# Performance work log

Hardware: AMD Instinct MI355X
Metric: run time of the kernel (lower is better)

Reference implementation:

```python
import jax, jax.numpy as jnp
import numpy as np

N, M, D = 1024, 1024, 512


def setup_inputs() -> dict:
    key = jax.random.key(0)
    ks = jax.random.split(key, 12)
    s = 1.0 / np.sqrt(D)
    return {
        "q": jax.random.normal(ks[0], (N, D), jnp.float32),
        "k": jax.random.normal(ks[1], (M, D), jnp.float32),
        "v": jax.random.normal(ks[2], (M, D), jnp.float32),
        "mask": jax.random.randint(ks[3], (N, M), 0, 2) > 0,
        "Wq": jax.random.normal(ks[4], (D, D), jnp.float32) * s,
        "bq": jax.random.normal(ks[5], (D,), jnp.float32) * s,
        "Wk": jax.random.normal(ks[6], (D, D), jnp.float32) * s,
        "bk": jax.random.normal(ks[7], (D,), jnp.float32) * s,
        "Wv": jax.random.normal(ks[8], (D, D), jnp.float32) * s,
        "bv": jax.random.normal(ks[9], (D,), jnp.float32) * s,
        "Ww": jax.random.normal(ks[10], (D,), jnp.float32) * s,
        "bw": jax.random.normal(ks[11], (1,), jnp.float32) * s,
    }


def reference(q, k, v, mask, Wq, bq, Wk, bk, Wv, bv, Ww, bw):
    # Linear projections (torch Linear: x @ W.T + b)
    qp = q @ Wq.T + bq  # [N, D]
    kp = k @ Wk.T + bk  # [M, D]
    vp = v @ Wv.T + bv  # [M, D]
    # Bahdanau additive score: W(tanh(q_n + k_m)) -> [N, M]
    h = jnp.tanh(qp[:, None, :] + kp[None, :, :])  # [N, M, D]
    scores = jnp.einsum('nmd,d->nm', h, Ww) + bw[0]
    scores = jnp.where(mask, scores, jnp.float32(-1000000.0))
    attn = jax.nn.softmax(scores, axis=1)  # softmax over M (dim 1)
    context = jnp.einsum('nm,md->nd', attn, vp)  # [N, D]
    return context
```

## Files before the change

### kernel.cpp

```cpp
#include <hip/hip_runtime.h>
#include <hip/hip_bf16.h>
#include <float.h>


#define NROWS 1024
#define DDIM  512
#define MDIM  1024

typedef __attribute__((ext_vector_type(8))) short s8v;
typedef __attribute__((ext_vector_type(4))) float f4v;
typedef __attribute__((ext_vector_type(2))) float v2f;

__device__ __forceinline__ float bf2f(ushort h) {
    return __uint_as_float(((unsigned)h) << 16);
}
__device__ __forceinline__ ushort2 f2bf2(float a, float b) {
    __hip_bfloat162 t = __float22bfloat162_rn(float2{a, b});
    union { __hip_bfloat162 v; ushort2 u; } c; c.v = t;
    return c.u;
}
__device__ __forceinline__ void hl2(float a, float b, ushort2& h, ushort2& l) {
    h = f2bf2(a, b);
    l = f2bf2(a - bf2f(h.x), b - bf2f(h.y));
}

__global__ __launch_bounds__(256) void proj_gemm(
    const float* __restrict__ q, const float* __restrict__ kk_,
    const float* __restrict__ v,
    const float* __restrict__ Wq, const float* __restrict__ bq,
    const float* __restrict__ Wk, const float* __restrict__ bk,
    const float* __restrict__ Wv, const float* __restrict__ bv,
    float* __restrict__ eq, float* __restrict__ ekT,
    ushort* __restrict__ vph, ushort* __restrict__ vpl,
    float* __restrict__ S, float CS)
{
    __shared__ ushort Ah[4096], Al[4096], Bh[4096], Bl[4096];

    const float* A; const float* B; const float* bias;
    int biasRow;
    if (blockIdx.z == 0)      { A = q;   B = Wq;  bias = bq; biasRow = 0; }
    else if (blockIdx.z == 1) { A = Wk;  B = kk_; bias = bk; biasRow = 1; }
    else                      { A = Wv;  B = v;   bias = bv; biasRow = 1; }

    const int bi = (blockIdx.z == 0) ? blockIdx.x : blockIdx.y;
    const int bj = (blockIdx.z == 0) ? blockIdx.y : blockIdx.x;

    const int t    = threadIdx.x;
    const int lane = t & 63;
    const int w    = t >> 6;
    const int lm   = lane & 15;
    const int lq   = lane >> 4;
    const int i0   = bi * 64;
    const int j0   = bj * 64;
    const int mh   = (w >> 1) * 32;
    const int nh   = (w & 1) * 32;

    if (blockIdx.z == 0) {
        const int jb = blockIdx.x * 8 + blockIdx.y;
        float4 zz = {0.f, 0.f, 0.f, 0.f};
#pragma unroll
        for (int p = 0; p < 8; ++p)
            *(float4*)&S[(size_t)jb * 8192 + (t + p * 256) * 4] = zz;
    }

    f4v acc[2][2] = {{{0.f,0.f,0.f,0.f},{0.f,0.f,0.f,0.f}},
                     {{0.f,0.f,0.f,0.f},{0.f,0.f,0.f,0.f}}};
    float4 pa[4], pb[4];

    const int sr = t >> 4, sc4 = t & 15;
#pragma unroll
    for (int p = 0; p < 4; ++p) {
        int r = sr + p * 16;
        pa[p] = *(const float4*)&A[(size_t)(i0 + r) * DDIM + sc4 * 4];
        pb[p] = *(const float4*)&B[(size_t)(j0 + r) * DDIM + sc4 * 4];
    }

    for (int kc = 0; kc < 8; ++kc) {
        __syncthreads();
#pragma unroll
        for (int p = 0; p < 4; ++p) {
            int r = sr + p * 16;
            int ad = r * 64 + (((sc4 >> 1) ^ (r & 7)) << 3) + (sc4 & 1) * 4;
            ushort2 h01, l01, h23, l23;
            hl2(pa[p].x, pa[p].y, h01, l01);
            hl2(pa[p].z, pa[p].w, h23, l23);
            ushort4 ha = {h01.x, h01.y, h23.x, h23.y};
            ushort4 la = {l01.x, l01.y, l23.x, l23.y};
            *(ushort4*)&Ah[ad] = ha;
            *(ushort4*)&Al[ad] = la;
            hl2(pb[p].x, pb[p].y, h01, l01);
            hl2(pb[p].z, pb[p].w, h23, l23);
            ushort4 hb = {h01.x, h01.y, h23.x, h23.y};
            ushort4 lb = {l01.x, l01.y, l23.x, l23.y};
            *(ushort4*)&Bh[ad] = hb;
            *(ushort4*)&Bl[ad] = lb;
        }
        __syncthreads();
        if (kc < 7) {
            const int k0 = (kc + 1) * 64;
#pragma unroll
            for (int p = 0; p < 4; ++p) {
                int r = sr + p * 16;
                pa[p] = *(const float4*)&A[(size_t)(i0 + r) * DDIM + k0 + sc4 * 4];
                pb[p] = *(const float4*)&B[(size_t)(j0 + r) * DDIM + k0 + sc4 * 4];
            }
        }
#pragma unroll
        for (int ks = 0; ks < 2; ++ks) {
            const int kb = ks * 4 + lq;
            s8v afh[2], afl[2], bfh[2], bfl[2];
#pragma unroll
            for (int g = 0; g < 2; ++g) {
                int ra = mh + g * 16 + lm;
                int rb = nh + g * 16 + lm;
                int aa = ra * 64 + ((kb ^ (ra & 7)) << 3);
                int ab = rb * 64 + ((kb ^ (rb & 7)) << 3);
                afh[g] = *(const s8v*)&Ah[aa];
                afl[g] = *(const s8v*)&Al[aa];
                bfh[g] = *(const s8v*)&Bh[ab];
                bfl[g] = *(const s8v*)&Bl[ab];
            }
#pragma unroll
            for (int mi = 0; mi < 2; ++mi)
#pragma unroll
                for (int ni = 0; ni < 2; ++ni) {
                    acc[mi][ni] = __builtin_amdgcn_mfma_f32_16x16x32_bf16(
                        afh[mi], bfh[ni], acc[mi][ni], 0, 0, 0);
                    acc[mi][ni] = __builtin_amdgcn_mfma_f32_16x16x32_bf16(
                        afh[mi], bfl[ni], acc[mi][ni], 0, 0, 0);
                    acc[mi][ni] = __builtin_amdgcn_mfma_f32_16x16x32_bf16(
                        afl[mi], bfh[ni], acc[mi][ni], 0, 0, 0);
                }
        }
    }

    const float CLAMP = 8192.0f;
    const float SCw   = 1.220703125e-4f;
#pragma unroll
    for (int mi = 0; mi < 2; ++mi) {
#pragma unroll
        for (int ni = 0; ni < 2; ++ni) {
#pragma unroll
            for (int p = 0; p < 4; ++p) {
                int row = i0 + mh + mi * 16 + lq * 4 + p;
                int col = j0 + nh + ni * 16 + lm;
                float val = acc[mi][ni][p] + (biasRow ? bias[row] : bias[col]);
                if (blockIdx.z == 0) {
                    eq[(size_t)row * 512 + col] =
                        fminf(__builtin_amdgcn_exp2f(val * CS), CLAMP) * SCw;
                } else if (blockIdx.z == 1) {
                    ekT[(size_t)row * 1024 + col] =
                        fminf(__builtin_amdgcn_exp2f(val * CS), CLAMP);
                } else {
                    ushort2 h2 = f2bf2(val, val);
                    vph[(size_t)row * 1024 + col] = h2.x;
                    ushort2 l2 = f2bf2(val - bf2f(h2.x), 0.f);
                    vpl[(size_t)row * 1024 + col] = l2.x;
                }
            }
        }
    }
}

#define SMCH 128

#define TREE8(K0,K1,K2,K3,K4,K5,K6,K7,DCQ)                                     \
    {                                                                          \
        float4 wgA = *(const float4*)&wws[(DCQ)];                              \
        float4 wgB = *(const float4*)&wws[(DCQ) + 4];                          \
        _Pragma("unroll")                                                      \
        for (int nn = 0; nn < 4; ++nn) {                                       \
            float4 egA = *(const float4*)&es[(wrow + nn) * 128 + (DCQ)];       \
            float4 egB = *(const float4*)&es[(wrow + nn) * 128 + (DCQ) + 4];   \
            v2f A0 = __builtin_elementwise_fma(K0, (v2f){egA.x, egA.x}, cc2);  \
            v2f A1 = __builtin_elementwise_fma(K1, (v2f){egA.y, egA.y}, cc2);  \
            v2f A2 = __builtin_elementwise_fma(K2, (v2f){egA.z, egA.z}, cc2);  \
            v2f A3 = __builtin_elementwise_fma(K3, (v2f){egA.w, egA.w}, cc2);  \
            v2f A4 = __builtin_elementwise_fma(K4, (v2f){egB.x, egB.x}, cc2);  \
            v2f A5 = __builtin_elementwise_fma(K5, (v2f){egB.y, egB.y}, cc2);  \
            v2f A6 = __builtin_elementwise_fma(K6, (v2f){egB.z, egB.z}, cc2);  \
            v2f A7 = __builtin_elementwise_fma(K7, (v2f){egB.w, egB.w}, cc2);  \
            v2f n01 = __builtin_elementwise_fma((v2f){wgA.y, wgA.y}, A0,       \
                                                (v2f){wgA.x, wgA.x} * A1);     \
            v2f d01 = A0 * A1;                                                 \
            v2f n23 = __builtin_elementwise_fma((v2f){wgA.w, wgA.w}, A2,       \
                                                (v2f){wgA.z, wgA.z} * A3);     \
            v2f d23 = A2 * A3;                                                 \
            v2f n45 = __builtin_elementwise_fma((v2f){wgB.y, wgB.y}, A4,       \
                                                (v2f){wgB.x, wgB.x} * A5);     \
            v2f d45 = A4 * A5;                                                 \
            v2f n67 = __builtin_elementwise_fma((v2f){wgB.w, wgB.w}, A6,       \
                                                (v2f){wgB.z, wgB.z} * A7);     \
            v2f d67 = A6 * A7;                                                 \
            v2f nA = __builtin_elementwise_fma(n01, d23, n23 * d01);           \
            v2f dA = d01 * d23;                                                \
            v2f nB = __builtin_elementwise_fma(n45, d67, n67 * d45);           \
            v2f dB = d45 * d67;                                                \
            v2f num = __builtin_elementwise_fma(nA, dB, nB * dA);              \
            v2f den = dA * dB;                                                 \
            v2f r = {__builtin_amdgcn_rcpf(den.x),                             \
                     __builtin_amdgcn_rcpf(den.y)};                            \
            acc[nn] = __builtin_elementwise_fma(num, r, acc[nn]);              \
        }                                                                      \
    }

__global__ __launch_bounds__(256) void score_kernel(const float* __restrict__ eq,
                                                    const float* __restrict__ ekT,
                                                    const float* __restrict__ Ww,
                                                    float* __restrict__ S)
{
    __shared__ __align__(16) float es[16 * 128];
    __shared__ __align__(16) float wws[128];
    const int t    = threadIdx.x;
    const int lane = t & 63;
    const int w    = t >> 6;
    const int m0   = blockIdx.x * SMCH;
    const int n0   = blockIdx.y * 16;
    const int dbase = blockIdx.z * 128;
    const int wrow = w * 4;

    const float SC = 1.220703125e-4f;

#pragma unroll
    for (int p = 0; p < 2; ++p) {
        int idx = t + p * 256;
        int nl = idx >> 5, dd4 = idx & 31;
        *(float4*)&es[nl * 128 + dd4 * 4] =
            *(const float4*)&eq[(size_t)(n0 + nl) * DDIM + dbase + dd4 * 4];
    }
    if (t < 128) wws[t] = Ww[dbase + t] * SC;

    const float* gk = ekT + (size_t)dbase * MDIM + m0 + lane * 2;

    v2f a0 = *(const v2f*)(gk + (size_t)0 * MDIM);
    v2f a1 = *(const v2f*)(gk + (size_t)1 * MDIM);
    v2f a2 = *(const v2f*)(gk + (size_t)2 * MDIM);
    v2f a3 = *(const v2f*)(gk + (size_t)3 * MDIM);
    v2f a4 = *(const v2f*)(gk + (size_t)4 * MDIM);
    v2f a5 = *(const v2f*)(gk + (size_t)5 * MDIM);
    v2f a6 = *(const v2f*)(gk + (size_t)6 * MDIM);
    v2f a7 = *(const v2f*)(gk + (size_t)7 * MDIM);

    __syncthreads();

    v2f acc[4] = {};
    const v2f cc2 = {1.220703125e-4f, 1.220703125e-4f};

    for (int dc = 0; dc < 128; dc += 16) {
        const float* g8 = gk + (size_t)(dc + 8) * MDIM;
        v2f b0 = *(const v2f*)(g8 + (size_t)0 * MDIM);
        v2f b1 = *(const v2f*)(g8 + (size_t)1 * MDIM);
        v2f b2 = *(const v2f*)(g8 + (size_t)2 * MDIM);
        v2f b3 = *(const v2f*)(g8 + (size_t)3 * MDIM);
        v2f b4 = *(const v2f*)(g8 + (size_t)4 * MDIM);
        v2f b5 = *(const v2f*)(g8 + (size_t)5 * MDIM);
        v2f b6 = *(const v2f*)(g8 + (size_t)6 * MDIM);
        v2f b7 = *(const v2f*)(g8 + (size_t)7 * MDIM);

        TREE8(a0, a1, a2, a3, a4, a5, a6, a7, dc)

        if (dc + 16 < 128) {
            const float* g16 = gk + (size_t)(dc + 16) * MDIM;
            a0 = *(const v2f*)(g16 + (size_t)0 * MDIM);
            a1 = *(const v2f*)(g16 + (size_t)1 * MDIM);
            a2 = *(const v2f*)(g16 + (size_t)2 * MDIM);
            a3 = *(const v2f*)(g16 + (size_t)3 * MDIM);
            a4 = *(const v2f*)(g16 + (size_t)4 * MDIM);
            a5 = *(const v2f*)(g16 + (size_t)5 * MDIM);
            a6 = *(const v2f*)(g16 + (size_t)6 * MDIM);
            a7 = *(const v2f*)(g16 + (size_t)7 * MDIM);
        }

        TREE8(b0, b1, b2, b3, b4, b5, b6, b7, dc + 8)
    }

    const float C2 = -2.8853900817779268f;
    const int m = m0 + lane * 2;
#pragma unroll
    for (int nn = 0; nn < 4; ++nn) {
        int n = n0 + wrow + nn;
        atomicAdd(&S[(size_t)n * MDIM + m],     acc[nn].x * C2);
        atomicAdd(&S[(size_t)n * MDIM + m + 1], acc[nn].y * C2);
    }
}

__global__ __launch_bounds__(256) void combine_kernel(const float* __restrict__ S,
                                                      const int* __restrict__ mask,
                                                      ushort* __restrict__ Ph,
                                                      ushort* __restrict__ Pl,
                                                      float* __restrict__ rsum)
{
    __shared__ float red[4];
    const int n = blockIdx.x, t = threadIdx.x;
    const int lane = t & 63, w = t >> 6;

    float4 s  = *(const float4*)&S[(size_t)n * MDIM + t * 4];
    int4   mk = *(const int4*)&mask[(size_t)n * MDIM + t * 4];
    float p0 = mk.x ? __builtin_amdgcn_exp2f(s.x) : 0.f;
    float p1 = mk.y ? __builtin_amdgcn_exp2f(s.y) : 0.f;
    float p2 = mk.z ? __builtin_amdgcn_exp2f(s.z) : 0.f;
    float p3 = mk.w ? __builtin_amdgcn_exp2f(s.w) : 0.f;

    ushort2 h01, l01, h23, l23;
    hl2(p0, p1, h01, l01);
    hl2(p2, p3, h23, l23);
    ushort4 hv = {h01.x, h01.y, h23.x, h23.y};
    ushort4 lv = {l01.x, l01.y, l23.x, l23.y};
    *(ushort4*)&Ph[(size_t)n * MDIM + t * 4] = hv;
    *(ushort4*)&Pl[(size_t)n * MDIM + t * 4] = lv;

    float rs = (p0 + p1) + (p2 + p3);
#pragma unroll
    for (int off = 32; off; off >>= 1) rs += __shfl_xor(rs, off);
    if (lane == 0) red[w] = rs;
    __syncthreads();
    if (t == 0) rsum[n] = (red[0] + red[1]) + (red[2] + red[3]);
}

__global__ __launch_bounds__(256) void ctx_gemm(const ushort* __restrict__ Ph,
                                                const ushort* __restrict__ Pl,
                                                const ushort* __restrict__ vph,
                                                const ushort* __restrict__ vpl,
                                                const float* __restrict__ rsum,
                                                float* __restrict__ out)
{
    __shared__ __align__(16) float red[3 * 64 * 4];
    const int t    = threadIdx.x;
    const int lane = t & 63;
    const int w    = t >> 6;
    const int lm   = lane & 15;
    const int lq   = lane >> 4;
    const int d0   = blockIdx.x * 16;
    const int n0   = blockIdx.y * 16;
    const int mb   = w * 256;

    const ushort* pAh = Ph  + (size_t)(n0 + lm) * MDIM + mb + lq * 8;
    const ushort* pAl = Pl  + (size_t)(n0 + lm) * MDIM + mb + lq * 8;
    const ushort* pBh = vph + (size_t)(d0 + lm) * MDIM + mb + lq * 8;
    const ushort* pBl = vpl + (size_t)(d0 + lm) * MDIM + mb + lq * 8;

    f4v acc = {0.f, 0.f, 0.f, 0.f};
#pragma unroll 4
    for (int m0 = 0; m0 < 256; m0 += 32) {
        s8v ah = *(const s8v*)(pAh + m0);
        s8v al = *(const s8v*)(pAl + m0);
        s8v bh = *(const s8v*)(pBh + m0);
        s8v bl = *(const s8v*)(pBl + m0);
        acc = __builtin_amdgcn_mfma_f32_16x16x32_bf16(ah, bh, acc, 0, 0, 0);
        acc = __builtin_amdgcn_mfma_f32_16x16x32_bf16(ah, bl, acc, 0, 0, 0);
        acc = __builtin_amdgcn_mfma_f32_16x16x32_bf16(al, bh, acc, 0, 0, 0);
    }

    if (w > 0) *(f4v*)&red[((w - 1) * 64 + lane) * 4] = acc;
    __syncthreads();
    if (w == 0) {
#pragma unroll
        for (int i = 0; i < 3; ++i)
            acc += *(const f4v*)&red[(i * 64 + lane) * 4];
#pragma unroll
        for (int p = 0; p < 4; ++p) {
            int nrow = n0 + lq * 4 + p;
            float inv = __builtin_amdgcn_rcpf(rsum[nrow]);
            out[(size_t)nrow * DDIM + d0 + lm] = acc[p] * inv;
        }
    }
}

extern "C" void kernel_launch(void* const* d_in, const int* in_sizes, int n_in,
                              void* d_out, int out_size, void* d_ws, size_t ws_size,
                              hipStream_t stream)
{
    const float* q    = (const float*)d_in[0];
    const float* k    = (const float*)d_in[1];
    const float* v    = (const float*)d_in[2];
    const int*   mask = (const int*)d_in[3];
    const float* Wq   = (const float*)d_in[4];
    const float* bq   = (const float*)d_in[5];
    const float* Wk   = (const float*)d_in[6];
    const float* bk   = (const float*)d_in[7];
    const float* Wv   = (const float*)d_in[8];
    const float* bv   = (const float*)d_in[9];
    const float* Ww   = (const float*)d_in[10];

    float* ws    = (float*)d_ws;
    float* eq    = ws;
    float* ekT   = ws + 524288;
    ushort* vph  = (ushort*)(ws + 1048576);
    ushort* vpl  = (ushort*)(ws + 1310720);
    float* S     = ws + 1572864;
    float* rsum  = ws + 2621440;
    ushort* Ph   = (ushort*)ws;
    ushort* Pl   = (ushort*)(ws + 524288);
    float* out   = (float*)d_out;

    const float CS = 2.8853900817779268f;

    proj_gemm<<<dim3(16, 8, 3), dim3(256), 0, stream>>>(q, k, v, Wq, bq, Wk, bk,
                                                        Wv, bv, eq, ekT,
                                                        vph, vpl, S, CS);
    score_kernel<<<dim3(8, 64, 4), dim3(256), 0, stream>>>(eq, ekT, Ww, S);
    combine_kernel<<<dim3(1024), dim3(256), 0, stream>>>(S, mask, Ph, Pl, rsum);
    ctx_gemm<<<dim3(32, 64), dim3(256), 0, stream>>>(Ph, Pl, vph, vpl, rsum, out);
}
```

Measured before the change: 179.9 us.

## Fuse softmax combine into score kernel by removing D-split and atomics

Score kernel now processes full D=512 per block for 4 rows (one per wave), so scores no longer need atomic accumulation into a global S buffer. The mask, exp2, bf16 hi/lo split and row-sum are done in the score epilogue, eliminating combine_kernel, the S zeroing, and S traffic. Row sums are accumulated via per-wave atomics into rsum, zeroed in proj_gemm. In exchange each ekT register load is reused across one row instead of four, increasing L2 reads and reducing per-thread ILP.

```diff
diff --git a/kernel.cpp b/kernel.cpp
--- a/kernel.cpp
+++ b/kernel.cpp
@@ -32,7 +32,7 @@
     const float* __restrict__ Wv, const float* __restrict__ bv,
     float* __restrict__ eq, float* __restrict__ ekT,
     ushort* __restrict__ vph, ushort* __restrict__ vpl,
-    float* __restrict__ S, float CS)
+    float* __restrict__ rsum, float CS)
 {
     __shared__ ushort Ah[4096], Al[4096], Bh[4096], Bl[4096];
 
@@ -55,12 +55,9 @@
     const int mh   = (w >> 1) * 32;
     const int nh   = (w & 1) * 32;
 
-    if (blockIdx.z == 0) {
-        const int jb = blockIdx.x * 8 + blockIdx.y;
+    if (blockIdx.z == 0 && blockIdx.x == 0 && blockIdx.y == 0) {
         float4 zz = {0.f, 0.f, 0.f, 0.f};
-#pragma unroll
-        for (int p = 0; p < 8; ++p)
-            *(float4*)&S[(size_t)jb * 8192 + (t + p * 256) * 4] = zz;
+        *(float4*)&rsum[t * 4] = zz;
     }
 
     f4v acc[2][2] = {{{0.f,0.f,0.f,0.f},{0.f,0.f,0.f,0.f}},
@@ -168,69 +165,68 @@
     {                                                                          \
         float4 wgA = *(const float4*)&wws[(DCQ)];                              \
         float4 wgB = *(const float4*)&wws[(DCQ) + 4];                          \
-        _Pragma("unroll")                                                      \
-        for (int nn = 0; nn < 4; ++nn) {                                       \
-            float4 egA = *(const float4*)&es[(wrow + nn) * 128 + (DCQ)];       \
-            float4 egB = *(const float4*)&es[(wrow + nn) * 128 + (DCQ) + 4];   \
-            v2f A0 = __builtin_elementwise_fma(K0, (v2f){egA.x, egA.x}, cc2);  \
-            v2f A1 = __builtin_elementwise_fma(K1, (v2f){egA.y, egA.y}, cc2);  \
-            v2f A2 = __builtin_elementwise_fma(K2, (v2f){egA.z, egA.z}, cc2);  \
-            v2f A3 = __builtin_elementwise_fma(K3, (v2f){egA.w, egA.w}, cc2);  \
-            v2f A4 = __builtin_elementwise_fma(K4, (v2f){egB.x, egB.x}, cc2);  \
-            v2f A5 = __builtin_elementwise_fma(K5, (v2f){egB.y, egB.y}, cc2);  \
-            v2f A6 = __builtin_elementwise_fma(K6, (v2f){egB.z, egB.z}, cc2);  \
-            v2f A7 = __builtin_elementwise_fma(K7, (v2f){egB.w, egB.w}, cc2);  \
-            v2f n01 = __builtin_elementwise_fma((v2f){wgA.y, wgA.y}, A0,       \
-                                                (v2f){wgA.x, wgA.x} * A1);     \
-            v2f d01 = A0 * A1;                                                 \
-            v2f n23 = __builtin_elementwise_fma((v2f){wgA.w, wgA.w}, A2,       \
-                                                (v2f){wgA.z, wgA.z} * A3);     \
-            v2f d23 = A2 * A3;                                                 \
-            v2f n45 = __builtin_elementwise_fma((v2f){wgB.y, wgB.y}, A4,       \
-                                                (v2f){wgB.x, wgB.x} * A5);     \
-            v2f d45 = A4 * A5;                                                 \
-            v2f n67 = __builtin_elementwise_fma((v2f){wgB.w, wgB.w}, A6,       \
-                                                (v2f){wgB.z, wgB.z} * A7);     \
-            v2f d67 = A6 * A7;                                                 \
-            v2f nA = __builtin_elementwise_fma(n01, d23, n23 * d01);           \
-            v2f dA = d01 * d23;                                                \
-            v2f nB = __builtin_elementwise_fma(n45, d67, n67 * d45);           \
-            v2f dB = d45 * d67;                                                \
-            v2f num = __builtin_elementwise_fma(nA, dB, nB * dA);              \
-            v2f den = dA * dB;                                                 \
-            v2f r = {__builtin_amdgcn_rcpf(den.x),                             \
-                     __builtin_amdgcn_rcpf(den.y)};                            \
-            acc[nn] = __builtin_elementwise_fma(num, r, acc[nn]);              \
-        }                                                                      \
+        float4 egA = *(const float4*)&esw[(DCQ)];                              \
+        float4 egB = *(const float4*)&esw[(DCQ) + 4];                          \
+        v2f A0 = __builtin_elementwise_fma(K0, (v2f){egA.x, egA.x}, cc2);      \
+        v2f A1 = __builtin_elementwise_fma(K1, (v2f){egA.y, egA.y}, cc2);      \
+        v2f A2 = __builtin_elementwise_fma(K2, (v2f){egA.z, egA.z}, cc2);      \
+        v2f A3 = __builtin_elementwise_fma(K3, (v2f){egA.w, egA.w}, cc2);      \
+        v2f A4 = __builtin_elementwise_fma(K4, (v2f){egB.x, egB.x}, cc2);      \
+        v2f A5 = __builtin_elementwise_fma(K5, (v2f){egB.y, egB.y}, cc2);      \
+        v2f A6 = __builtin_elementwise_fma(K6, (v2f){egB.z, egB.z}, cc2);      \
+        v2f A7 = __builtin_elementwise_fma(K7, (v2f){egB.w, egB.w}, cc2);      \
+        v2f n01 = __builtin_elementwise_fma((v2f){wgA.y, wgA.y}, A0,           \
+                                            (v2f){wgA.x, wgA.x} * A1);         \
+        v2f d01 = A0 * A1;                                                     \
+        v2f n23 = __builtin_elementwise_fma((v2f){wgA.w, wgA.w}, A2,           \
+                                            (v2f){wgA.z, wgA.z} * A3);         \
+        v2f d23 = A2 * A3;                                                     \
+        v2f n45 = __builtin_elementwise_fma((v2f){wgB.y, wgB.y}, A4,           \
+                                            (v2f){wgB.x, wgB.x} * A5);         \
+        v2f d45 = A4 * A5;                                                     \
+        v2f n67 = __builtin_elementwise_fma((v2f){wgB.w, wgB.w}, A6,           \
+                                            (v2f){wgB.z, wgB.z} * A7);         \
+        v2f d67 = A6 * A7;                                                     \
+        v2f nA = __builtin_elementwise_fma(n01, d23, n23 * d01);               \
+        v2f dA = d01 * d23;                                                    \
+        v2f nB = __builtin_elementwise_fma(n45, d67, n67 * d45);               \
+        v2f dB = d45 * d67;                                                    \
+        v2f num = __builtin_elementwise_fma(nA, dB, nB * dA);                  \
+        v2f den = dA * dB;                                                     \
+        v2f r = {__builtin_amdgcn_rcpf(den.x),                                 \
+                 __builtin_amdgcn_rcpf(den.y)};                                \
+        acc = __builtin_elementwise_fma(num, r, acc);                          \
     }
 
 __global__ __launch_bounds__(256) void score_kernel(const float* __restrict__ eq,
                                                     const float* __restrict__ ekT,
                                                     const float* __restrict__ Ww,
-                                                    float* __restrict__ S)
+                                                    const int* __restrict__ mask,
+                                                    ushort* __restrict__ Ph,
+                                                    ushort* __restrict__ Pl,
+                                                    float* __restrict__ rsum)
 {
-    __shared__ __align__(16) float es[16 * 128];
-    __shared__ __align__(16) float wws[128];
+    __shared__ __align__(16) float es[4 * 512];
+    __shared__ __align__(16) float wws[512];
     const int t    = threadIdx.x;
     const int lane = t & 63;
     const int w    = t >> 6;
     const int m0   = blockIdx.x * SMCH;
-    const int n0   = blockIdx.y * 16;
-    const int dbase = blockIdx.z * 128;
-    const int wrow = w * 4;
+    const int n0   = blockIdx.y * 4;
 
     const float SC = 1.220703125e-4f;
 
 #pragma unroll
     for (int p = 0; p < 2; ++p) {
         int idx = t + p * 256;
-        int nl = idx >> 5, dd4 = idx & 31;
-        *(float4*)&es[nl * 128 + dd4 * 4] =
-            *(const float4*)&eq[(size_t)(n0 + nl) * DDIM + dbase + dd4 * 4];
-    }
-    if (t < 128) wws[t] = Ww[dbase + t] * SC;
-
-    const float* gk = ekT + (size_t)dbase * MDIM + m0 + lane * 2;
+        int nl = idx >> 7, c4 = idx & 127;
+        *(float4*)&es[nl * 512 + c4 * 4] =
+            *(const float4*)&eq[(size_t)(n0 + nl) * DDIM + c4 * 4];
+    }
+    wws[t]       = Ww[t] * SC;
+    wws[t + 256] = Ww[t + 256] * SC;
+
+    const float* gk = ekT + m0 + lane * 2;
 
     v2f a0 = *(const v2f*)(gk + (size_t)0 * MDIM);
     v2f a1 = *(const v2f*)(gk + (size_t)1 * MDIM);
@@ -243,10 +239,11 @@
 
     __syncthreads();
 
-    v2f acc[4] = {};
+    const float* esw = &es[w * 512];
+    v2f acc = {0.f, 0.f};
     const v2f cc2 = {1.220703125e-4f, 1.220703125e-4f};
 
-    for (int dc = 0; dc < 128; dc += 16) {
+    for (int dc = 0; dc < 512; dc += 16) {
         const float* g8 = gk + (size_t)(dc + 8) * MDIM;
         v2f b0 = *(const v2f*)(g8 + (size_t)0 * MDIM);
         v2f b1 = *(const v2f*)(g8 + (size_t)1 * MDIM);
@@ -259,7 +256,7 @@
 
         TREE8(a0, a1, a2, a3, a4, a5, a6, a7, dc)
 
-        if (dc + 16 < 128) {
+        if (dc + 16 < 512) {
             const float* g16 = gk + (size_t)(dc + 16) * MDIM;
             a0 = *(const v2f*)(g16 + (size_t)0 * MDIM);
             a1 = *(const v2f*)(g16 + (size_t)1 * MDIM);
@@ -275,46 +272,21 @@
     }
 
     const float C2 = -2.8853900817779268f;
+    const int n = n0 + w;
     const int m = m0 + lane * 2;
-#pragma unroll
-    for (int nn = 0; nn < 4; ++nn) {
-        int n = n0 + wrow + nn;
-        atomicAdd(&S[(size_t)n * MDIM + m],     acc[nn].x * C2);
-        atomicAdd(&S[(size_t)n * MDIM + m + 1], acc[nn].y * C2);
-    }
-}
-
-__global__ __launch_bounds__(256) void combine_kernel(const float* __restrict__ S,
-                                                      const int* __restrict__ mask,
-                                                      ushort* __restrict__ Ph,
-                                                      ushort* __restrict__ Pl,
-                                                      float* __restrict__ rsum)
-{
-    __shared__ float red[4];
-    const int n = blockIdx.x, t = threadIdx.x;
-    const int lane = t & 63, w = t >> 6;
-
-    float4 s  = *(const float4*)&S[(size_t)n * MDIM + t * 4];
-    int4   mk = *(const int4*)&mask[(size_t)n * MDIM + t * 4];
-    float p0 = mk.x ? __builtin_amdgcn_exp2f(s.x) : 0.f;
-    float p1 = mk.y ? __builtin_amdgcn_exp2f(s.y) : 0.f;
-    float p2 = mk.z ? __builtin_amdgcn_exp2f(s.z) : 0.f;
-    float p3 = mk.w ? __builtin_amdgcn_exp2f(s.w) : 0.f;
-
-    ushort2 h01, l01, h23, l23;
-    hl2(p0, p1, h01, l01);
-    hl2(p2, p3, h23, l23);
-    ushort4 hv = {h01.x, h01.y, h23.x, h23.y};
-    ushort4 lv = {l01.x, l01.y, l23.x, l23.y};
-    *(ushort4*)&Ph[(size_t)n * MDIM + t * 4] = hv;
-    *(ushort4*)&Pl[(size_t)n * MDIM + t * 4] = lv;
-
-    float rs = (p0 + p1) + (p2 + p3);
+    int2 mk = *(const int2*)&mask[(size_t)n * MDIM + m];
+    float p0 = mk.x ? __builtin_amdgcn_exp2f(acc.x * C2) : 0.f;
+    float p1 = mk.y ? __builtin_amdgcn_exp2f(acc.y * C2) : 0.f;
+
+    ushort2 h, l;
+    hl2(p0, p1, h, l);
+    *(ushort2*)&Ph[(size_t)n * MDIM + m] = h;
+    *(ushort2*)&Pl[(size_t)n * MDIM + m] = l;
+
+    float rs = p0 + p1;
 #pragma unroll
     for (int off = 32; off; off >>= 1) rs += __shfl_xor(rs, off);
-    if (lane == 0) red[w] = rs;
-    __syncthreads();
-    if (t == 0) rsum[n] = (red[0] + red[1]) + (red[2] + red[3]);
+    if (lane == 0) atomicAdd(&rsum[n], rs);
 }
 
 __global__ __launch_bounds__(256) void ctx_gemm(const ushort* __restrict__ Ph,
@@ -387,18 +359,17 @@
     float* ekT   = ws + 524288;
     ushort* vph  = (ushort*)(ws + 1048576);
     ushort* vpl  = (ushort*)(ws + 1310720);
-    float* S     = ws + 1572864;
+    ushort* Ph   = (ushort*)(ws + 1572864);
+    ushort* Pl   = (ushort*)(ws + 2097152);
     float* rsum  = ws + 2621440;
-    ushort* Ph   = (ushort*)ws;
-    ushort* Pl   = (ushort*)(ws + 524288);
     float* out   = (float*)d_out;
 
     const float CS = 2.8853900817779268f;
 
     proj_gemm<<<dim3(16, 8, 3), dim3(256), 0, stream>>>(q, k, v, Wq, bq, Wk, bk,
                                                         Wv, bv, eq, ekT,
-                                                        vph, vpl, S, CS);
-    score_kernel<<<dim3(8, 64, 4), dim3(256), 0, stream>>>(eq, ekT, Ww, S);
-    combine_kernel<<<dim3(1024), dim3(256), 0, stream>>>(S, mask, Ph, Pl, rsum);
+                                                        vph, vpl, rsum, CS);
+    score_kernel<<<dim3(8, 256), dim3(256), 0, stream>>>(eq, ekT, Ww, mask,
+                                                         Ph, Pl, rsum);
     ctx_gemm<<<dim3(32, 64), dim3(256), 0, stream>>>(Ph, Pl, vph, vpl, rsum, out);
 }
```

New measurement: 242.3 us. 34.7% more time.

## Fuse softmax combine into score kernel by looping full D per block

Applied to the files above, without the earlier changes.

The score kernel now processes the whole 512-wide D dimension per block instead of splitting D across four z-blocks. Each thread therefore holds complete scores and can apply the mask, exp, bf16 hi/lo split and row-sum directly, which removes the S scratch buffer, its zeroing, the float atomics on S and the separate combine kernel. Row sums are still accumulated with one atomic per wavefront per row, so rsum is zeroed in proj_gemm. The grid shrinks from 2048 to 512 blocks with four times the inner-loop length, which lowers parallelism and latency hiding.

```diff
diff --git a/kernel.cpp b/kernel.cpp
--- a/kernel.cpp
+++ b/kernel.cpp
@@ -32,7 +32,7 @@
     const float* __restrict__ Wv, const float* __restrict__ bv,
     float* __restrict__ eq, float* __restrict__ ekT,
     ushort* __restrict__ vph, ushort* __restrict__ vpl,
-    float* __restrict__ S, float CS)
+    float* __restrict__ rsum, float CS)
 {
     __shared__ ushort Ah[4096], Al[4096], Bh[4096], Bl[4096];
 
@@ -55,12 +55,9 @@
     const int mh   = (w >> 1) * 32;
     const int nh   = (w & 1) * 32;
 
-    if (blockIdx.z == 0) {
-        const int jb = blockIdx.x * 8 + blockIdx.y;
+    if (blockIdx.z == 0 && blockIdx.x == 0 && blockIdx.y == 0) {
         float4 zz = {0.f, 0.f, 0.f, 0.f};
-#pragma unroll
-        for (int p = 0; p < 8; ++p)
-            *(float4*)&S[(size_t)jb * 8192 + (t + p * 256) * 4] = zz;
+        *(float4*)&rsum[t * 4] = zz;
     }
 
     f4v acc[2][2] = {{{0.f,0.f,0.f,0.f},{0.f,0.f,0.f,0.f}},
@@ -162,7 +159,6 @@
     }
 }
 
-#define SMCH 128
 
 #define TREE8(K0,K1,K2,K3,K4,K5,K6,K7,DCQ)                                     \
     {                                                                          \
@@ -170,8 +166,8 @@
         float4 wgB = *(const float4*)&wws[(DCQ) + 4];                          \
         _Pragma("unroll")                                                      \
         for (int nn = 0; nn < 4; ++nn) {                                       \
-            float4 egA = *(const float4*)&es[(wrow + nn) * 128 + (DCQ)];       \
-            float4 egB = *(const float4*)&es[(wrow + nn) * 128 + (DCQ) + 4];   \
+            float4 egA = *(const float4*)&es[nn * 512 + (DCQ)];                \
+            float4 egB = *(const float4*)&es[nn * 512 + (DCQ) + 4];            \
             v2f A0 = __builtin_elementwise_fma(K0, (v2f){egA.x, egA.x}, cc2);  \
             v2f A1 = __builtin_elementwise_fma(K1, (v2f){egA.y, egA.y}, cc2);  \
             v2f A2 = __builtin_elementwise_fma(K2, (v2f){egA.z, egA.z}, cc2);  \
@@ -207,30 +203,32 @@
 __global__ __launch_bounds__(256) void score_kernel(const float* __restrict__ eq,
                                                     const float* __restrict__ ekT,
                                                     const float* __restrict__ Ww,
-                                                    float* __restrict__ S)
+                                                    const int* __restrict__ mask,
+                                                    ushort* __restrict__ Ph,
+                                                    ushort* __restrict__ Pl,
+                                                    float* __restrict__ rsum)
 {
-    __shared__ __align__(16) float es[16 * 128];
-    __shared__ __align__(16) float wws[128];
+    __shared__ __align__(16) float es[4 * 512];
+    __shared__ __align__(16) float wws[512];
     const int t    = threadIdx.x;
     const int lane = t & 63;
     const int w    = t >> 6;
-    const int m0   = blockIdx.x * SMCH;
-    const int n0   = blockIdx.y * 16;
-    const int dbase = blockIdx.z * 128;
-    const int wrow = w * 4;
+    const int mw   = blockIdx.x * 512 + w * 128;
+    const int n0   = blockIdx.y * 4;
 
     const float SC = 1.220703125e-4f;
 
 #pragma unroll
     for (int p = 0; p < 2; ++p) {
         int idx = t + p * 256;
-        int nl = idx >> 5, dd4 = idx & 31;
-        *(float4*)&es[nl * 128 + dd4 * 4] =
-            *(const float4*)&eq[(size_t)(n0 + nl) * DDIM + dbase + dd4 * 4];
-    }
-    if (t < 128) wws[t] = Ww[dbase + t] * SC;
-
-    const float* gk = ekT + (size_t)dbase * MDIM + m0 + lane * 2;
+        int nl = idx >> 7, c4 = idx & 127;
+        *(float4*)&es[nl * 512 + c4 * 4] =
+            *(const float4*)&eq[(size_t)(n0 + nl) * DDIM + c4 * 4];
+    }
+    wws[t]       = Ww[t] * SC;
+    wws[t + 256] = Ww[t + 256] * SC;
+
+    const float* gk = ekT + mw + lane * 2;
 
     v2f a0 = *(const v2f*)(gk + (size_t)0 * MDIM);
     v2f a1 = *(const v2f*)(gk + (size_t)1 * MDIM);
@@ -246,7 +244,7 @@
     v2f acc[4] = {};
     const v2f cc2 = {1.220703125e-4f, 1.220703125e-4f};
 
-    for (int dc = 0; dc < 128; dc += 16) {
+    for (int dc = 0; dc < 512; dc += 16) {
         const float* g8 = gk + (size_t)(dc + 8) * MDIM;
         v2f b0 = *(const v2f*)(g8 + (size_t)0 * MDIM);
         v2f b1 = *(const v2f*)(g8 + (size_t)1 * MDIM);
@@ -259,7 +257,7 @@
 
         TREE8(a0, a1, a2, a3, a4, a5, a6, a7, dc)
 
-        if (dc + 16 < 128) {
+        if (dc + 16 < 512) {
             const float* g16 = gk + (size_t)(dc + 16) * MDIM;
             a0 = *(const v2f*)(g16 + (size_t)0 * MDIM);
             a1 = *(const v2f*)(g16 + (size_t)1 * MDIM);
@@ -275,46 +273,32 @@
     }
 
     const float C2 = -2.8853900817779268f;
-    const int m = m0 + lane * 2;
+    const int m = mw + lane * 2;
+    float rs[4];
 #pragma unroll
     for (int nn = 0; nn < 4; ++nn) {
-        int n = n0 + wrow + nn;
-        atomicAdd(&S[(size_t)n * MDIM + m],     acc[nn].x * C2);
-        atomicAdd(&S[(size_t)n * MDIM + m + 1], acc[nn].y * C2);
-    }
-}
-
-__global__ __launch_bounds__(256) void combine_kernel(const float* __restrict__ S,
-                                                      const int* __restrict__ mask,
-                                                      ushort* __restrict__ Ph,
-                                                      ushort* __restrict__ Pl,
-                                                      float* __restrict__ rsum)
-{
-    __shared__ float red[4];
-    const int n = blockIdx.x, t = threadIdx.x;
-    const int lane = t & 63, w = t >> 6;
-
-    float4 s  = *(const float4*)&S[(size_t)n * MDIM + t * 4];
-    int4   mk = *(const int4*)&mask[(size_t)n * MDIM + t * 4];
-    float p0 = mk.x ? __builtin_amdgcn_exp2f(s.x) : 0.f;
-    float p1 = mk.y ? __builtin_amdgcn_exp2f(s.y) : 0.f;
-    float p2 = mk.z ? __builtin_amdgcn_exp2f(s.z) : 0.f;
-    float p3 = mk.w ? __builtin_amdgcn_exp2f(s.w) : 0.f;
-
-    ushort2 h01, l01, h23, l23;
-    hl2(p0, p1, h01, l01);
-    hl2(p2, p3, h23, l23);
-    ushort4 hv = {h01.x, h01.y, h23.x, h23.y};
-    ushort4 lv = {l01.x, l01.y, l23.x, l23.y};
-    *(ushort4*)&Ph[(size_t)n * MDIM + t * 4] = hv;
-    *(ushort4*)&Pl[(size_t)n * MDIM + t * 4] = lv;
-
-    float rs = (p0 + p1) + (p2 + p3);
-#pragma unroll
-    for (int off = 32; off; off >>= 1) rs += __shfl_xor(rs, off);
-    if (lane == 0) red[w] = rs;
-    __syncthreads();
-    if (t == 0) rsum[n] = (red[0] + red[1]) + (red[2] + red[3]);
+        int n = n0 + nn;
+        int2 mk = *(const int2*)&mask[(size_t)n * MDIM + m];
+        float p0 = mk.x ? __builtin_amdgcn_exp2f(acc[nn].x * C2) : 0.f;
+        float p1 = mk.y ? __builtin_amdgcn_exp2f(acc[nn].y * C2) : 0.f;
+        ushort2 h, l;
+        hl2(p0, p1, h, l);
+        *(ushort2*)&Ph[(size_t)n * MDIM + m] = h;
+        *(ushort2*)&Pl[(size_t)n * MDIM + m] = l;
+        rs[nn] = p0 + p1;
+    }
+#pragma unroll
+    for (int off = 32; off; off >>= 1) {
+        rs[0] += __shfl_xor(rs[0], off);
+        rs[1] += __shfl_xor(rs[1], off);
+        rs[2] += __shfl_xor(rs[2], off);
+        rs[3] += __shfl_xor(rs[3], off);
+    }
+    if (lane == 0) {
+#pragma unroll
+        for (int nn = 0; nn < 4; ++nn)
+            atomicAdd(&rsum[n0 + nn], rs[nn]);
+    }
 }
 
 __global__ __launch_bounds__(256) void ctx_gemm(const ushort* __restrict__ Ph,
@@ -387,18 +371,17 @@
     float* ekT   = ws + 524288;
     ushort* vph  = (ushort*)(ws + 1048576);
     ushort* vpl  = (ushort*)(ws + 1310720);
-    float* S     = ws + 1572864;
+    ushort* Ph   = (ushort*)(ws + 1572864);
+    ushort* Pl   = (ushort*)(ws + 2097152);
     float* rsum  = ws + 2621440;
-    ushort* Ph   = (ushort*)ws;
-    ushort* Pl   = (ushort*)(ws + 524288);
     float* out   = (float*)d_out;
 
     const float CS = 2.8853900817779268f;
 
     proj_gemm<<<dim3(16, 8, 3), dim3(256), 0, stream>>>(q, k, v, Wq, bq, Wk, bk,
                                                         Wv, bv, eq, ekT,
-                                                        vph, vpl, S, CS);
-    score_kernel<<<dim3(8, 64, 4), dim3(256), 0, stream>>>(eq, ekT, Ww, S);
-    combine_kernel<<<dim3(1024), dim3(256), 0, stream>>>(S, mask, Ph, Pl, rsum);
+                                                        vph, vpl, rsum, CS);
+    score_kernel<<<dim3(2, 256), dim3(256), 0, stream>>>(eq, ekT, Ww, mask,
+                                                         Ph, Pl, rsum);
     ctx_gemm<<<dim3(32, 64), dim3(256), 0, stream>>>(Ph, Pl, vph, vpl, rsum, out);
 }
```

New measurement: 176.1 us. -2.1%, faster.
